# Optimization experiments

Hardware: AMD Instinct MI355X
Metric: run time of the kernel (lower is better)

The kernel has to match this reference:

```python
import jax, jax.numpy as jnp
import numpy as np

B, N, C = 8, 4096, 768
H, HD = 12, 64          # num_heads, head_dim = C // H
M = HD * 2              # rand_feat_dim
LAM = 0.3
NUM_STEP = 5


def setup_inputs() -> dict:
    key = jax.random.key(0)
    k1, k2, k3, k4 = jax.random.split(key, 4)
    x = jax.random.normal(k1, (B, N, C), dtype=jnp.float32)
    Wqkv = jax.random.normal(k2, (C, 2 * C), dtype=jnp.float32) * 0.02
    Wproj = jax.random.normal(k3, (C, C), dtype=jnp.float32) * 0.02
    bproj = jnp.zeros((C,), dtype=jnp.float32)
    rand_matrix = jax.random.normal(k4, (H, HD, M), dtype=jnp.float32)
    return {"x": x, "Wqkv": Wqkv, "Wproj": Wproj, "bproj": bproj,
            "rand_matrix": rand_matrix}


def _soft(z, t):
    # sign(z) * relu(|z| - t): soft-thresholding (ISTA proximal step)
    return jnp.sign(z) * jax.nn.relu(jnp.abs(z) - t)


def reference(x, Wqkv, Wproj, bproj, rand_matrix):
    Bn, Nn, Cn = x.shape
    Hh, hd, m = rand_matrix.shape
    scale = hd ** (-0.5)

    qkv = x @ Wqkv                                   # [B,N,2C]
    q = qkv[..., :Cn].reshape(Bn, Nn, Hh, hd).transpose(0, 2, 1, 3)  # [B,H,N,hd]
    v = qkv[..., Cn:].reshape(Bn, Nn, Hh, hd).transpose(0, 2, 1, 3)  # [B,H,N,hd]

    # random-feature map: exp(q @ proj - ||q||^2 / 2) / sqrt(m)
    qs = q * scale ** 0.5
    rf = jnp.exp(jnp.einsum('bhnd,hdm->bhnm', qs, rand_matrix)
                 - 0.5 * jnp.sum(qs * qs, axis=-1, keepdims=True)) / m ** 0.5
    # F.normalize(p=2, dim=-2): normalize over the sequence axis
    qn = rf / jnp.maximum(jnp.linalg.norm(rf, axis=-2, keepdims=True), 1e-12)

    kk = jnp.einsum('bhnm,bhnp->bhmp', qn, qn)       # [B,H,m,m]
    kv = jnp.einsum('bhnm,bhnd->bhmd', qn, v)        # [B,H,m,hd]

    # Lipschitz bound: max row L1 norm of kk, detached
    L = jax.lax.stop_gradient(
        jnp.max(jnp.sum(jnp.abs(kk), axis=-1), axis=-1))[..., None, None] + 1.0

    # unrolled ISTA soft-thresholding loop
    s = _soft(kv, LAM)
    for _ in range(NUM_STEP):
        s = _soft(s - (kk @ s - kv) / L, LAM / L)

    out = jnp.einsum('bhnm,bhmd->bhnd', qn, s)       # [B,H,N,hd]
    out = out.transpose(0, 2, 1, 3).reshape(Bn, Nn, Cn)
    return out @ Wproj + bproj
```

## Files before the change

kernel.cpp:

```cpp
#include <hip/hip_runtime.h>


typedef __attribute__((ext_vector_type(8))) short bf16x8;
typedef __attribute__((ext_vector_type(4))) float f32x4;

#define GLD16(gptr, lptr)                                                              \
  __builtin_amdgcn_global_load_lds((const __attribute__((address_space(1))) void*)(gptr), \
                                   (__attribute__((address_space(3))) void*)(lptr), 16, 0, 0)

__device__ __forceinline__ unsigned short f2bf(float f) {
  union { float f; unsigned int u; } v; v.f = f;
  unsigned int r = v.u + 0x7fffu + ((v.u >> 16) & 1u);
  return (unsigned short)(r >> 16);
}
__device__ __forceinline__ float bf2f(unsigned short s) {
  union { unsigned int u; float f; } v; v.u = ((unsigned int)s) << 16;
  return v.f;
}
__device__ __forceinline__ float rn_of(float css) {
  return 1.f / fmaxf(sqrtf(css), 1e-12f);
}

template<int BM, int BN>
__device__ __forceinline__ void gemm_core_nt(
    const unsigned short* __restrict__ A, int lda,
    const unsigned short* __restrict__ B0,
    const unsigned short* __restrict__ B1, int brows0, int ldb,
    int K,
    f32x4 (&acc)[BM / 32][BN / 32],
    unsigned short* As, unsigned short* Bs) {
  constexpr int MT = BM / 32, NT = BN / 32;
  const int tid = threadIdx.x;
  const int lane = tid & 63, wave = tid >> 6;
  const int wm = (wave >> 1) * (BM / 2), wn = (wave & 1) * (BN / 2);
  const int l16 = lane & 15, quad = lane >> 4;
  const int arow = tid >> 2, ako = (tid & 3) << 3;
#pragma unroll
  for (int i = 0; i < MT; i++)
#pragma unroll
    for (int j = 0; j < NT; j++)
#pragma unroll
      for (int r = 0; r < 4; r++) acc[i][j][r] = 0.f;

  for (int k0 = 0; k0 < K; k0 += 32) {
    __syncthreads();
#pragma unroll
    for (int c = 0; c < BM / 64; c++) {
      const unsigned short* gp = A + (long)(arow + c * 64) * lda + k0 + ako;
      GLD16(gp, As + (c * 256 + wave * 64) * 8);
    }
#pragma unroll
    for (int c = 0; c < BN / 64; c++) {
      int row = arow + c * 64;
      const unsigned short* bp = (row < brows0) ? (B0 + (long)row * ldb)
                                                : (B1 + (long)(row - brows0) * ldb);
      GLD16(bp + k0 + ako, Bs + (c * 256 + wave * 64) * 8);
    }
    __syncthreads();
    bf16x8 af[MT], bfr[NT];
#pragma unroll
    for (int i = 0; i < MT; i++)
      af[i] = *(const bf16x8*)(As + (wm + i * 16 + l16) * 32 + quad * 8);
#pragma unroll
    for (int j = 0; j < NT; j++)
      bfr[j] = *(const bf16x8*)(Bs + (wn + j * 16 + l16) * 32 + quad * 8);
#pragma unroll
    for (int i = 0; i < MT; i++)
#pragma unroll
      for (int j = 0; j < NT; j++)
        acc[i][j] = __builtin_amdgcn_mfma_f32_16x16x32_bf16(af[i], bfr[j], acc[i][j], 0, 0, 0);
  }
}

__global__ __launch_bounds__(256) void k_convert_bf16(const float* __restrict__ in,
                                                      unsigned short* __restrict__ out, long n4) {
  long i = (long)blockIdx.x * 256 + threadIdx.x;
  if (i < n4) {
    float4 v = ((const float4*)in)[i];
    unsigned short o[4] = {f2bf(v.x), f2bf(v.y), f2bf(v.z), f2bf(v.w)};
    ((uint2*)out)[i] = *(uint2*)o;
  }
}

__global__ __launch_bounds__(256) void k_transpose_bf16(const float* __restrict__ in,
                                                        unsigned short* __restrict__ out,
                                                        int R, int C, float scale) {
  int b = blockIdx.y;
  long base = (long)b * R * C;
  long idx = (long)blockIdx.x * 256 + threadIdx.x;
  if (idx < (long)R * C) {
    int oc = (int)(idx / R);
    int orr = (int)(idx - (long)oc * R);
    out[base + idx] = f2bf(in[base + (long)orr * C + oc] * scale);
  }
}

__global__ __launch_bounds__(256) void k_gemm_qkv(const unsigned short* __restrict__ xbf,
                                                  const unsigned short* __restrict__ wqkvT,
                                                  unsigned short* __restrict__ q,
                                                  unsigned short* __restrict__ vT) {
  __shared__ __align__(16) unsigned short pool[8576];
  unsigned short* As = pool;
  unsigned short* Bs = pool + 4096;
  f32x4 acc[4][4];
  const int L = blockIdx.x;
  const int xcd = L & 7, slot = L >> 3;
  const int rt = xcd * 32 + slot / 12;
  const int ct = slot % 12;
  const int tid = threadIdx.x, lane = tid & 63, wave = tid >> 6;
  const int l16 = lane & 15, quad = lane >> 4;
  const int wm = (wave >> 1) * 64, wn = (wave & 1) * 64;

  const unsigned short* A = xbf + (long)rt * 128 * 768;
  const unsigned short* B = wqkvT + (long)ct * 128 * 768;
  gemm_core_nt<128, 128>(A, 768, B, B, 128, 768, 768, acc, As, Bs);

  const int b = rt >> 5;
  const int nbase = (rt & 31) * 128;
  if (ct < 6) {
#pragma unroll
    for (int i = 0; i < 4; i++)
#pragma unroll
      for (int j = 0; j < 4; j++)
#pragma unroll
        for (int r = 0; r < 4; r++) {
          int col = ct * 128 + wn + j * 16 + l16;
          int h = col >> 6, d = col & 63;
          int n = nbase + wm + i * 16 + quad * 4 + r;
          q[((long)(b * 12 + h) * 4096 + n) * 64 + d] = f2bf(acc[i][j][r]);
        }
  } else {
    for (int hh = 0; hh < 2; hh++) {
      __syncthreads();
      if ((wave >> 1) == hh) {
#pragma unroll
        for (int i = 0; i < 4; i++)
#pragma unroll
          for (int j = 0; j < 4; j++)
#pragma unroll
            for (int r = 0; r < 4; r++)
              pool[(i * 16 + quad * 4 + r) * 134 + wn + j * 16 + l16] = f2bf(acc[i][j][r]);
      }
      __syncthreads();
#pragma unroll
      for (int c = 0; c < 4; c++) {
        int chunk = tid + c * 256;
        int col = chunk >> 3, nj = (chunk & 7) * 8;
        unsigned short o[8];
#pragma unroll
        for (int e = 0; e < 8; e++) o[e] = pool[(nj + e) * 134 + col];
        int vcol = ct * 128 - 768 + col;
        int h = vcol >> 6, d = vcol & 63;
        long n = nbase + hh * 64 + nj;
        *(uint4*)&vT[((long)(b * 12 + h) * 64 + d) * 4096 + n] = *(uint4*)o;
      }
    }
  }
}

__global__ __launch_bounds__(256) void k_gemm_rf(const unsigned short* __restrict__ q,
                                                 const unsigned short* __restrict__ rmT,
                                                 unsigned short* __restrict__ qnT,
                                                 float* __restrict__ colss) {
  __shared__ __align__(16) unsigned short smem[16384];
  __shared__ float hnp[256];
  __shared__ float css[128];
  unsigned short* Asm = smem;
  unsigned short* Bsm = smem + 8192;
  unsigned short* pool = smem;
  f32x4 acc[4][4];
  const int nt = blockIdx.x, bh = blockIdx.y, h = bh % 12;
  const int tid = threadIdx.x, lane = tid & 63, wave = tid >> 6;
  const int l16 = lane & 15, quad = lane >> 4;
  const int wm = (wave >> 1) * 64, wn = (wave & 1) * 64;
  const unsigned short* Aq = q + ((long)bh * 4096 + nt * 128) * 64;
  const unsigned short* Brm = rmT + (long)h * 8192;

#pragma unroll
  for (int c = 0; c < 4; c++) {
    int chunk = c * 256 + tid;
    int row = chunk >> 3, ko8 = chunk & 7;
    int kc = ko8 >> 2, kw = (ko8 & 3) * 8;
    *(uint4*)(Asm + kc * 4096 + row * 32 + kw) = *(const uint4*)(Aq + (long)row * 64 + ko8 * 8);
    *(uint4*)(Bsm + kc * 4096 + row * 32 + kw) = *(const uint4*)(Brm + (long)row * 64 + ko8 * 8);
  }
  for (int i = tid; i < 128; i += 256) css[i] = 0.f;
  __syncthreads();
  {
    const unsigned short* ap = Asm + (tid & 1) * 4096 + (tid >> 1) * 32;
    float ssum = 0.f;
#pragma unroll
    for (int e = 0; e < 32; e++) { float f = bf2f(ap[e]); ssum += f * f; }
    hnp[tid] = ssum;
  }
#pragma unroll
  for (int i = 0; i < 4; i++)
#pragma unroll
    for (int j = 0; j < 4; j++)
#pragma unroll
      for (int r = 0; r < 4; r++) acc[i][j][r] = 0.f;
#pragma unroll
  for (int kc = 0; kc < 2; kc++) {
    bf16x8 af[4], bfr[4];
#pragma unroll
    for (int i = 0; i < 4; i++)
      af[i] = *(const bf16x8*)(Asm + kc * 4096 + (wm + i * 16 + l16) * 32 + quad * 8);
#pragma unroll
    for (int j = 0; j < 4; j++)
      bfr[j] = *(const bf16x8*)(Bsm + kc * 4096 + (wn + j * 16 + l16) * 32 + quad * 8);
#pragma unroll
    for (int i = 0; i < 4; i++)
#pragma unroll
      for (int j = 0; j < 4; j++)
        acc[i][j] = __builtin_amdgcn_mfma_f32_16x16x32_bf16(af[i], bfr[j], acc[i][j], 0, 0, 0);
  }
  __syncthreads();
  float hnv[4][4];
#pragma unroll
  for (int i = 0; i < 4; i++)
#pragma unroll
    for (int r = 0; r < 4; r++) {
      int row = wm + i * 16 + quad * 4 + r;
      hnv[i][r] = 0.0625f * (hnp[2 * row] + hnp[2 * row + 1]);
    }
#pragma unroll
  for (int j = 0; j < 4; j++) {
    int col = wn + j * 16 + l16;
    float cp = 0.f;
#pragma unroll
    for (int i = 0; i < 4; i++)
#pragma unroll
      for (int r = 0; r < 4; r++) {
        float v = __expf(acc[i][j][r] - hnv[i][r]) * 0.08838834764831845f;
        acc[i][j][r] = v;
        cp += v * v;
      }
    atomicAdd(&css[col], cp);
  }
  __syncthreads();
  for (int i = tid; i < 128; i += 256) atomicAdd(&colss[bh * 128 + i], css[i]);
  for (int hh = 0; hh < 2; hh++) {
    __syncthreads();
    if ((wave >> 1) == hh) {
#pragma unroll
      for (int i = 0; i < 4; i++)
#pragma unroll
        for (int j = 0; j < 4; j++)
#pragma unroll
          for (int r = 0; r < 4; r++)
            pool[(i * 16 + quad * 4 + r) * 134 + wn + j * 16 + l16] = f2bf(acc[i][j][r]);
    }
    __syncthreads();
#pragma unroll
    for (int c = 0; c < 4; c++) {
      int chunk = tid + c * 256;
      int m = chunk >> 3, nj = (chunk & 7) * 8;
      unsigned short o[8];
#pragma unroll
      for (int e = 0; e < 8; e++) o[e] = pool[(nj + e) * 134 + m];
      *(uint4*)&qnT[((long)bh * 128 + m) * 4096 + nt * 128 + hh * 64 + nj] = *(uint4*)o;
    }
  }
}

__global__ __launch_bounds__(256) void k_gemm_kkkv(const unsigned short* __restrict__ qnT,
                                                   const unsigned short* __restrict__ vT,
                                                   const float* __restrict__ colss,
                                                   float* __restrict__ kkkv) {
  __shared__ __align__(16) unsigned short As[128 * 32], Bs[192 * 32];
  f32x4 acc[4][6];
  const int ks = blockIdx.x, bh = blockIdx.y;
  const unsigned short* A = qnT + (long)bh * 128 * 4096 + ks * 512;
  const unsigned short* B1 = vT + (long)bh * 64 * 4096 + ks * 512;
  gemm_core_nt<128, 192>(A, 4096, A, B1, 128, 4096, 512, acc, As, Bs);
  const int lane = threadIdx.x & 63, wave = threadIdx.x >> 6;
  const int l16 = lane & 15, quad = lane >> 4;
  const int wm = (wave >> 1) * 64, wn = (wave & 1) * 96;
  float rnr[4][4];
#pragma unroll
  for (int i = 0; i < 4; i++)
#pragma unroll
    for (int r = 0; r < 4; r++)
      rnr[i][r] = rn_of(colss[bh * 128 + wm + i * 16 + quad * 4 + r]);
#pragma unroll
  for (int j = 0; j < 6; j++) {
    int col = wn + j * 16 + l16;
    float rnc = (col < 128) ? rn_of(colss[bh * 128 + col]) : 1.f;
#pragma unroll
    for (int i = 0; i < 4; i++)
#pragma unroll
      for (int r = 0; r < 4; r++) {
        int row = wm + i * 16 + quad * 4 + r;
        atomicAdd(&kkkv[((long)bh * 128 + row) * 192 + col], acc[i][j][r] * rnr[i][r] * rnc);
      }
  }
}

__global__ __launch_bounds__(256) void k_ista(const float* __restrict__ kkkv,
                                              const float* __restrict__ colss,
                                              unsigned short* __restrict__ sT) {
  __shared__ __align__(16) unsigned short kks[128 * 144];
  __shared__ __align__(16) unsigned short ssT[64 * 144];
  __shared__ float red[128];
  __shared__ float rns[128];
  const int tid = threadIdx.x, lane = tid & 63, wave = tid >> 6;
  const int l16 = lane & 15, quad = lane >> 4;
  const int wm = (wave >> 1) * 64, wn = (wave & 1) * 32;
  const int bh = blockIdx.x;
  const float* kkb = kkkv + (long)bh * 128 * 192;
  for (int idx = tid; idx < 128 * 32; idx += 256) {
    int m = idx >> 5, p4 = (idx & 31) * 4;
    float4 v = *(const float4*)(kkb + (long)m * 192 + p4);
    unsigned short o[4] = {f2bf(v.x), f2bf(v.y), f2bf(v.z), f2bf(v.w)};
    *(uint2*)(kks + m * 144 + p4) = *(uint2*)o;
  }
  float kv[4][2][4];
#pragma unroll
  for (int i = 0; i < 4; i++)
#pragma unroll
    for (int j = 0; j < 2; j++)
#pragma unroll
      for (int r = 0; r < 4; r++) {
        int m = wm + i * 16 + quad * 4 + r, d = wn + j * 16 + l16;
        kv[i][j][r] = kkb[(long)m * 192 + 128 + d];
      }
  __syncthreads();
  if (tid < 128) {
    float rs = 0.f;
    const unsigned short* rp = kks + tid * 144;
    for (int p = 0; p < 128; p++) rs += fabsf(bf2f(rp[p]));
    red[tid] = rs;
    rns[tid] = rn_of(colss[bh * 128 + tid]);
  }
  __syncthreads();
  for (int o = 64; o > 0; o >>= 1) {
    if (tid < o) red[tid] = fmaxf(red[tid], red[tid + o]);
    __syncthreads();
  }
  const float L = red[0] + 1.f;
  const float invL = 1.f / L;
  const float lamL = 0.3f * invL;
  float sreg[4][2][4];
#pragma unroll
  for (int i = 0; i < 4; i++)
#pragma unroll
    for (int j = 0; j < 2; j++)
#pragma unroll
      for (int r = 0; r < 4; r++) {
        float z = kv[i][j][r];
        float az = fabsf(z) - 0.3f;
        float s = az > 0.f ? copysignf(az, z) : 0.f;
        sreg[i][j][r] = s;
        ssT[(wn + j * 16 + l16) * 144 + wm + i * 16 + quad * 4 + r] = f2bf(s);
      }
  for (int step = 0; step < 5; step++) {
    __syncthreads();
    f32x4 acc[4][2];
#pragma unroll
    for (int i = 0; i < 4; i++)
#pragma unroll
      for (int j = 0; j < 2; j++)
#pragma unroll
        for (int r = 0; r < 4; r++) acc[i][j][r] = 0.f;
#pragma unroll
    for (int kc = 0; kc < 4; kc++) {
      bf16x8 af[4], bfj[2];
#pragma unroll
      for (int i = 0; i < 4; i++)
        af[i] = *(const bf16x8*)(kks + (wm + i * 16 + l16) * 144 + kc * 32 + quad * 8);
#pragma unroll
      for (int j = 0; j < 2; j++)
        bfj[j] = *(const bf16x8*)(ssT + (wn + j * 16 + l16) * 144 + kc * 32 + quad * 8);
#pragma unroll
      for (int i = 0; i < 4; i++)
#pragma unroll
        for (int j = 0; j < 2; j++)
          acc[i][j] = __builtin_amdgcn_mfma_f32_16x16x32_bf16(af[i], bfj[j], acc[i][j], 0, 0, 0);
    }
    __syncthreads();
#pragma unroll
    for (int i = 0; i < 4; i++)
#pragma unroll
      for (int j = 0; j < 2; j++)
#pragma unroll
        for (int r = 0; r < 4; r++) {
          float z = sreg[i][j][r] - (acc[i][j][r] - kv[i][j][r]) * invL;
          float az = fabsf(z) - lamL;
          float s = az > 0.f ? copysignf(az, z) : 0.f;
          sreg[i][j][r] = s;
          ssT[(wn + j * 16 + l16) * 144 + wm + i * 16 + quad * 4 + r] = f2bf(s);
        }
  }
#pragma unroll
  for (int i = 0; i < 4; i++)
#pragma unroll
    for (int j = 0; j < 2; j++)
#pragma unroll
      for (int r = 0; r < 4; r++) {
        int m = wm + i * 16 + quad * 4 + r, d = wn + j * 16 + l16;
        sT[(long)bh * 8192 + d * 128 + m] = f2bf(sreg[i][j][r] * rns[m]);
      }
}

__global__ __launch_bounds__(256) void k_gemm_attn(const unsigned short* __restrict__ qnT,
                                                   const unsigned short* __restrict__ sT,
                                                   unsigned short* __restrict__ attn) {
  __shared__ __align__(16) unsigned short As2[32 * 128];
  __shared__ __align__(16) unsigned short Bs[64 * 32];
  f32x4 acc[4][2];
  const int nt = blockIdx.x, bh = blockIdx.y;
  const int b = bh / 12, h = bh % 12;
  const int tid = threadIdx.x, lane = tid & 63, wave = tid >> 6;
  const int l16 = lane & 15, quad = lane >> 4;
  const int wm = (wave >> 1) * 64, wn = (wave & 1) * 32;
#pragma unroll
  for (int i = 0; i < 4; i++)
#pragma unroll
    for (int j = 0; j < 2; j++)
#pragma unroll
      for (int r = 0; r < 4; r++) acc[i][j][r] = 0.f;
  for (int k0 = 0; k0 < 128; k0 += 32) {
    __syncthreads();
#pragma unroll
    for (int c = 0; c < 2; c++) {
      int chunk = tid + c * 256;
      int kr = chunk >> 4, n0 = (chunk & 15) * 8;
      const unsigned short* gp = qnT + ((long)bh * 128 + k0 + kr) * 4096 + nt * 128 + n0;
      GLD16(gp, As2 + (c * 256 + wave * 64) * 8);
    }
    {
      int dd = tid >> 2, ko = (tid & 3) * 8;
      const unsigned short* gp = sT + ((long)bh * 64 + dd) * 128 + k0 + ko;
      GLD16(gp, Bs + wave * 512);
    }
    __syncthreads();
    bf16x8 af[4], bfr[2];
#pragma unroll
    for (int i = 0; i < 4; i++) {
      union { bf16x8 v; unsigned short s[8]; } u;
#pragma unroll
      for (int e = 0; e < 8; e++) u.s[e] = As2[(quad * 8 + e) * 128 + wm + i * 16 + l16];
      af[i] = u.v;
    }
#pragma unroll
    for (int j = 0; j < 2; j++)
      bfr[j] = *(const bf16x8*)&Bs[(wn + j * 16 + l16) * 32 + quad * 8];
#pragma unroll
    for (int i = 0; i < 4; i++)
#pragma unroll
      for (int j = 0; j < 2; j++)
        acc[i][j] = __builtin_amdgcn_mfma_f32_16x16x32_bf16(af[i], bfr[j], acc[i][j], 0, 0, 0);
  }
#pragma unroll
  for (int i = 0; i < 4; i++)
#pragma unroll
    for (int j = 0; j < 2; j++)
#pragma unroll
      for (int r = 0; r < 4; r++) {
        int n = nt * 128 + wm + i * 16 + quad * 4 + r;
        int dd = wn + j * 16 + l16;
        attn[((long)b * 4096 + n) * 768 + h * 64 + dd] = f2bf(acc[i][j][r]);
      }
}

__global__ __launch_bounds__(256) void k_gemm_proj(const unsigned short* __restrict__ attn,
                                                   const unsigned short* __restrict__ wprojT,
                                                   const float* __restrict__ bias,
                                                   float* __restrict__ out) {
  __shared__ __align__(16) unsigned short As[128 * 32], Bs[128 * 32];
  f32x4 acc[4][4];
  const int Lb = blockIdx.x;
  const int xcd = Lb & 7, slot = Lb >> 3;
  const int rt = xcd * 32 + slot / 6;
  const int ct = slot % 6;
  const unsigned short* A = attn + (long)rt * 128 * 768;
  const unsigned short* B = wprojT + (long)ct * 128 * 768;
  gemm_core_nt<128, 128>(A, 768, B, B, 128, 768, 768, acc, As, Bs);
  const int lane = threadIdx.x & 63, wave = threadIdx.x >> 6;
  const int l16 = lane & 15, quad = lane >> 4;
  const int wm = (wave >> 1) * 64, wn = (wave & 1) * 64;
  long row0 = (long)rt * 128, col0 = (long)ct * 128;
#pragma unroll
  for (int i = 0; i < 4; i++)
#pragma unroll
    for (int j = 0; j < 4; j++) {
      int col = (int)col0 + wn + j * 16 + l16;
      float bv = bias[col];
#pragma unroll
      for (int r = 0; r < 4; r++) {
        long row = row0 + wm + i * 16 + quad * 4 + r;
        out[row * 768 + col] = acc[i][j][r] + bv;
      }
    }
}

extern "C" void kernel_launch(void* const* d_in, const int* in_sizes, int n_in,
                              void* d_out, int out_size, void* d_ws, size_t ws_size,
                              hipStream_t stream) {
  const float* x = (const float*)d_in[0];
  const float* Wqkv = (const float*)d_in[1];
  const float* Wproj = (const float*)d_in[2];
  const float* bproj = (const float*)d_in[3];
  const float* rm = (const float*)d_in[4];
  float* out = (float*)d_out;

  size_t o = 0;
  char* wsb = (char*)d_ws;
  auto take = [&](size_t b) { char* p = wsb + o; o += b; return p; };
  unsigned short* wqkvT = (unsigned short*)take(2359296);
  unsigned short* wprojT = (unsigned short*)take(1179648);
  unsigned short* rmT = (unsigned short*)take(196608);
  unsigned short* q = (unsigned short*)take(50331648);
  unsigned short* vT = (unsigned short*)take(50331648);
  float* colss = (float*)take(49152);
  float* kkkv = (float*)take(9437184);
  unsigned short* sT = (unsigned short*)take(1572864);
  if (ws_size < o) return;

  unsigned short* xbf = (unsigned short*)d_out;
  unsigned short* qnT = (unsigned short*)d_out;
  unsigned short* attnbf = q;

  hipMemsetAsync(colss, 0, 49152, stream);
  hipMemsetAsync(kkkv, 0, 9437184, stream);

  k_convert_bf16<<<24576, 256, 0, stream>>>(x, xbf, 6291456L);
  k_transpose_bf16<<<dim3(4608, 1), 256, 0, stream>>>(Wqkv, wqkvT, 768, 1536, 1.0f);
  k_transpose_bf16<<<dim3(2304, 1), 256, 0, stream>>>(Wproj, wprojT, 768, 768, 1.0f);
  k_transpose_bf16<<<dim3(32, 12), 256, 0, stream>>>(rm, rmT, 64, 128, 0.3535533905932738f);
  k_gemm_qkv<<<3072, 256, 0, stream>>>(xbf, wqkvT, q, vT);
  k_gemm_rf<<<dim3(32, 96), 256, 0, stream>>>(q, rmT, qnT, colss);
  k_gemm_kkkv<<<dim3(8, 96), 256, 0, stream>>>(qnT, vT, colss, kkkv);
  k_ista<<<96, 256, 0, stream>>>(kkkv, colss, sT);
  k_gemm_attn<<<dim3(32, 96), 256, 0, stream>>>(qnT, sT, attnbf);
  k_gemm_proj<<<1536, 256, 0, stream>>>(attnbf, wprojT, bproj, out);
}
```

Baseline: 524.4 us.

## Swizzle LDS tiles, tile weight transposes, replace kk/kv atomics with partial-sum buffers

Applies an XOR swizzle to the 32-wide bf16 LDS tiles in the shared GEMM core, the rf GEMM and the attn GEMM to reduce bank conflicts on fragment reads. Replaces the strided element-wise weight transpose with a 32x32 shared-memory tiled transpose so both reads and writes are coalesced. Replaces float atomicAdd split-K accumulation of kk/kv with per-split bf16 partial buffers that the ISTA kernel sums, which also removes a memset. Partials stored in bf16 lose some precision before the reduction, and reusing the q buffer for them depends on q being dead by then.

```diff
diff --git a/kernel.cpp b/kernel.cpp
--- a/kernel.cpp
+++ b/kernel.cpp
@@ -34,7 +34,9 @@
   const int lane = tid & 63, wave = tid >> 6;
   const int wm = (wave >> 1) * (BM / 2), wn = (wave & 1) * (BN / 2);
   const int l16 = lane & 15, quad = lane >> 4;
-  const int arow = tid >> 2, ako = (tid & 3) << 3;
+  const int arow = tid >> 2;
+  const int akos = (((tid & 3) ^ ((arow >> 1) & 3)) << 3);
+  const int fsw = (l16 >> 1) & 3;
 #pragma unroll
   for (int i = 0; i < MT; i++)
 #pragma unroll
@@ -46,7 +48,7 @@
     __syncthreads();
 #pragma unroll
     for (int c = 0; c < BM / 64; c++) {
-      const unsigned short* gp = A + (long)(arow + c * 64) * lda + k0 + ako;
+      const unsigned short* gp = A + (long)(arow + c * 64) * lda + k0 + akos;
       GLD16(gp, As + (c * 256 + wave * 64) * 8);
     }
 #pragma unroll
@@ -54,16 +56,16 @@
       int row = arow + c * 64;
       const unsigned short* bp = (row < brows0) ? (B0 + (long)row * ldb)
                                                 : (B1 + (long)(row - brows0) * ldb);
-      GLD16(bp + k0 + ako, Bs + (c * 256 + wave * 64) * 8);
+      GLD16(bp + k0 + akos, Bs + (c * 256 + wave * 64) * 8);
     }
     __syncthreads();
     bf16x8 af[MT], bfr[NT];
 #pragma unroll
     for (int i = 0; i < MT; i++)
-      af[i] = *(const bf16x8*)(As + (wm + i * 16 + l16) * 32 + quad * 8);
+      af[i] = *(const bf16x8*)(As + (wm + i * 16 + l16) * 32 + ((quad ^ fsw) * 8));
 #pragma unroll
     for (int j = 0; j < NT; j++)
-      bfr[j] = *(const bf16x8*)(Bs + (wn + j * 16 + l16) * 32 + quad * 8);
+      bfr[j] = *(const bf16x8*)(Bs + (wn + j * 16 + l16) * 32 + ((quad ^ fsw) * 8));
 #pragma unroll
     for (int i = 0; i < MT; i++)
 #pragma unroll
@@ -82,17 +84,21 @@
   }
 }
 
-__global__ __launch_bounds__(256) void k_transpose_bf16(const float* __restrict__ in,
-                                                        unsigned short* __restrict__ out,
-                                                        int R, int C, float scale) {
-  int b = blockIdx.y;
-  long base = (long)b * R * C;
-  long idx = (long)blockIdx.x * 256 + threadIdx.x;
-  if (idx < (long)R * C) {
-    int oc = (int)(idx / R);
-    int orr = (int)(idx - (long)oc * R);
-    out[base + idx] = f2bf(in[base + (long)orr * C + oc] * scale);
-  }
+__global__ __launch_bounds__(256) void k_transpose_tiled(const float* __restrict__ in,
+                                                         unsigned short* __restrict__ out,
+                                                         int R, int C, float scale) {
+  __shared__ float t[32][33];
+  const float* ib = in + (long)blockIdx.z * R * C;
+  unsigned short* ob = out + (long)blockIdx.z * R * C;
+  int c0 = blockIdx.x * 32, r0 = blockIdx.y * 32;
+  int tx = threadIdx.x & 31, ty = threadIdx.x >> 5;
+#pragma unroll
+  for (int k = 0; k < 32; k += 8)
+    t[ty + k][tx] = ib[(long)(r0 + ty + k) * C + c0 + tx];
+  __syncthreads();
+#pragma unroll
+  for (int k = 0; k < 32; k += 8)
+    ob[(long)(c0 + ty + k) * R + r0 + tx] = f2bf(t[tx][ty + k] * scale);
 }
 
 __global__ __launch_bounds__(256) void k_gemm_qkv(const unsigned short* __restrict__ xbf,
@@ -173,6 +179,7 @@
   const int tid = threadIdx.x, lane = tid & 63, wave = tid >> 6;
   const int l16 = lane & 15, quad = lane >> 4;
   const int wm = (wave >> 1) * 64, wn = (wave & 1) * 64;
+  const int fsw = (l16 >> 1) & 3;
   const unsigned short* Aq = q + ((long)bh * 4096 + nt * 128) * 64;
   const unsigned short* Brm = rmT + (long)h * 8192;
 
@@ -180,9 +187,10 @@
   for (int c = 0; c < 4; c++) {
     int chunk = c * 256 + tid;
     int row = chunk >> 3, ko8 = chunk & 7;
-    int kc = ko8 >> 2, kw = (ko8 & 3) * 8;
-    *(uint4*)(Asm + kc * 4096 + row * 32 + kw) = *(const uint4*)(Aq + (long)row * 64 + ko8 * 8);
-    *(uint4*)(Bsm + kc * 4096 + row * 32 + kw) = *(const uint4*)(Brm + (long)row * 64 + ko8 * 8);
+    int kc = ko8 >> 2;
+    int c2s = (ko8 & 3) ^ ((row >> 1) & 3);
+    *(uint4*)(Asm + kc * 4096 + row * 32 + c2s * 8) = *(const uint4*)(Aq + (long)row * 64 + ko8 * 8);
+    *(uint4*)(Bsm + kc * 4096 + row * 32 + c2s * 8) = *(const uint4*)(Brm + (long)row * 64 + ko8 * 8);
   }
   for (int i = tid; i < 128; i += 256) css[i] = 0.f;
   __syncthreads();
@@ -204,10 +212,10 @@
     bf16x8 af[4], bfr[4];
 #pragma unroll
     for (int i = 0; i < 4; i++)
-      af[i] = *(const bf16x8*)(Asm + kc * 4096 + (wm + i * 16 + l16) * 32 + quad * 8);
+      af[i] = *(const bf16x8*)(Asm + kc * 4096 + (wm + i * 16 + l16) * 32 + ((quad ^ fsw) * 8));
 #pragma unroll
     for (int j = 0; j < 4; j++)
-      bfr[j] = *(const bf16x8*)(Bsm + kc * 4096 + (wn + j * 16 + l16) * 32 + quad * 8);
+      bfr[j] = *(const bf16x8*)(Bsm + kc * 4096 + (wn + j * 16 + l16) * 32 + ((quad ^ fsw) * 8));
 #pragma unroll
     for (int i = 0; i < 4; i++)
 #pragma unroll
@@ -266,7 +274,7 @@
 __global__ __launch_bounds__(256) void k_gemm_kkkv(const unsigned short* __restrict__ qnT,
                                                    const unsigned short* __restrict__ vT,
                                                    const float* __restrict__ colss,
-                                                   float* __restrict__ kkkv) {
+                                                   unsigned short* __restrict__ kkp) {
   __shared__ __align__(16) unsigned short As[128 * 32], Bs[192 * 32];
   f32x4 acc[4][6];
   const int ks = blockIdx.x, bh = blockIdx.y;
@@ -276,6 +284,7 @@
   const int lane = threadIdx.x & 63, wave = threadIdx.x >> 6;
   const int l16 = lane & 15, quad = lane >> 4;
   const int wm = (wave >> 1) * 64, wn = (wave & 1) * 96;
+  unsigned short* dst = kkp + ((long)ks * 96 + bh) * 24576;
   float rnr[4][4];
 #pragma unroll
   for (int i = 0; i < 4; i++)
@@ -291,29 +300,43 @@
 #pragma unroll
       for (int r = 0; r < 4; r++) {
         int row = wm + i * 16 + quad * 4 + r;
-        atomicAdd(&kkkv[((long)bh * 128 + row) * 192 + col], acc[i][j][r] * rnr[i][r] * rnc);
-      }
-  }
-}
-
-__global__ __launch_bounds__(256) void k_ista(const float* __restrict__ kkkv,
+        dst[row * 192 + col] = f2bf(acc[i][j][r] * rnr[i][r] * rnc);
+      }
+  }
+}
+
+__global__ __launch_bounds__(256) void k_ista(const unsigned short* __restrict__ kkp,
                                               const float* __restrict__ colss,
                                               unsigned short* __restrict__ sT) {
   __shared__ __align__(16) unsigned short kks[128 * 144];
   __shared__ __align__(16) unsigned short ssT[64 * 144];
+  __shared__ float kvs[128 * 64];
   __shared__ float red[128];
   __shared__ float rns[128];
   const int tid = threadIdx.x, lane = tid & 63, wave = tid >> 6;
   const int l16 = lane & 15, quad = lane >> 4;
   const int wm = (wave >> 1) * 64, wn = (wave & 1) * 32;
   const int bh = blockIdx.x;
-  const float* kkb = kkkv + (long)bh * 128 * 192;
-  for (int idx = tid; idx < 128 * 32; idx += 256) {
-    int m = idx >> 5, p4 = (idx & 31) * 4;
-    float4 v = *(const float4*)(kkb + (long)m * 192 + p4);
-    unsigned short o[4] = {f2bf(v.x), f2bf(v.y), f2bf(v.z), f2bf(v.w)};
-    *(uint2*)(kks + m * 144 + p4) = *(uint2*)o;
-  }
+  const unsigned short* base = kkp + (long)bh * 24576;
+  for (int idx = tid; idx < 3072; idx += 256) {
+    int m = idx / 24, c8 = idx % 24;
+    float f[8] = {0.f, 0.f, 0.f, 0.f, 0.f, 0.f, 0.f, 0.f};
+#pragma unroll
+    for (int ks = 0; ks < 8; ks++) {
+      union { uint4 u; unsigned short s[8]; } u;
+      u.u = *(const uint4*)(base + (long)ks * 2359296 + m * 192 + c8 * 8);
+#pragma unroll
+      for (int e = 0; e < 8; e++) f[e] += bf2f(u.s[e]);
+    }
+    if (c8 < 16) {
+#pragma unroll
+      for (int e = 0; e < 8; e++) kks[m * 144 + c8 * 8 + e] = f2bf(f[e]);
+    } else {
+#pragma unroll
+      for (int e = 0; e < 8; e++) kvs[m * 64 + (c8 - 16) * 8 + e] = f[e];
+    }
+  }
+  __syncthreads();
   float kv[4][2][4];
 #pragma unroll
   for (int i = 0; i < 4; i++)
@@ -322,9 +345,8 @@
 #pragma unroll
       for (int r = 0; r < 4; r++) {
         int m = wm + i * 16 + quad * 4 + r, d = wn + j * 16 + l16;
-        kv[i][j][r] = kkb[(long)m * 192 + 128 + d];
-      }
-  __syncthreads();
+        kv[i][j][r] = kvs[m * 64 + d];
+      }
   if (tid < 128) {
     float rs = 0.f;
     const unsigned short* rp = kks + tid * 144;
@@ -413,6 +435,7 @@
   const int tid = threadIdx.x, lane = tid & 63, wave = tid >> 6;
   const int l16 = lane & 15, quad = lane >> 4;
   const int wm = (wave >> 1) * 64, wn = (wave & 1) * 32;
+  const int fsw = (l16 >> 1) & 3;
 #pragma unroll
   for (int i = 0; i < 4; i++)
 #pragma unroll
@@ -429,7 +452,8 @@
       GLD16(gp, As2 + (c * 256 + wave * 64) * 8);
     }
     {
-      int dd = tid >> 2, ko = (tid & 3) * 8;
+      int dd = tid >> 2;
+      int ko = (((tid & 3) ^ ((dd >> 1) & 3)) * 8);
       const unsigned short* gp = sT + ((long)bh * 64 + dd) * 128 + k0 + ko;
       GLD16(gp, Bs + wave * 512);
     }
@@ -444,7 +468,7 @@
     }
 #pragma unroll
     for (int j = 0; j < 2; j++)
-      bfr[j] = *(const bf16x8*)&Bs[(wn + j * 16 + l16) * 32 + quad * 8];
+      bfr[j] = *(const bf16x8*)&Bs[(wn + j * 16 + l16) * 32 + ((quad ^ fsw) * 8)];
 #pragma unroll
     for (int i = 0; i < 4; i++)
 #pragma unroll
@@ -513,25 +537,24 @@
   unsigned short* q = (unsigned short*)take(50331648);
   unsigned short* vT = (unsigned short*)take(50331648);
   float* colss = (float*)take(49152);
-  float* kkkv = (float*)take(9437184);
   unsigned short* sT = (unsigned short*)take(1572864);
   if (ws_size < o) return;
 
   unsigned short* xbf = (unsigned short*)d_out;
   unsigned short* qnT = (unsigned short*)d_out;
+  unsigned short* kkp = q;
   unsigned short* attnbf = q;
 
   hipMemsetAsync(colss, 0, 49152, stream);
-  hipMemsetAsync(kkkv, 0, 9437184, stream);
 
   k_convert_bf16<<<24576, 256, 0, stream>>>(x, xbf, 6291456L);
-  k_transpose_bf16<<<dim3(4608, 1), 256, 0, stream>>>(Wqkv, wqkvT, 768, 1536, 1.0f);
-  k_transpose_bf16<<<dim3(2304, 1), 256, 0, stream>>>(Wproj, wprojT, 768, 768, 1.0f);
-  k_transpose_bf16<<<dim3(32, 12), 256, 0, stream>>>(rm, rmT, 64, 128, 0.3535533905932738f);
+  k_transpose_tiled<<<dim3(48, 24, 1), 256, 0, stream>>>(Wqkv, wqkvT, 768, 1536, 1.0f);
+  k_transpose_tiled<<<dim3(24, 24, 1), 256, 0, stream>>>(Wproj, wprojT, 768, 768, 1.0f);
+  k_transpose_tiled<<<dim3(4, 2, 12), 256, 0, stream>>>(rm, rmT, 64, 128, 0.3535533905932738f);
   k_gemm_qkv<<<3072, 256, 0, stream>>>(xbf, wqkvT, q, vT);
   k_gemm_rf<<<dim3(32, 96), 256, 0, stream>>>(q, rmT, qnT, colss);
-  k_gemm_kkkv<<<dim3(8, 96), 256, 0, stream>>>(qnT, vT, colss, kkkv);
-  k_ista<<<96, 256, 0, stream>>>(kkkv, colss, sT);
+  k_gemm_kkkv<<<dim3(8, 96), 256, 0, stream>>>(qnT, vT, colss, kkp);
+  k_ista<<<96, 256, 0, stream>>>(kkp, colss, sT);
   k_gemm_attn<<<dim3(32, 96), 256, 0, stream>>>(qnT, sT, attnbf);
   k_gemm_proj<<<1536, 256, 0, stream>>>(attnbf, wprojT, bproj, out);
 }
```

Result: faster. 478.5 us (-8.8%).
